# Kernel tuning notes

Hardware: AMD Instinct MI355X
Metric: run time of the kernel (lower is better)

Reference implementation:

```python
import jax, jax.numpy as jnp
import numpy as np

B, T, S, NH, MD, FF, H = 2, 4096, 4096, 16, 64, 128, 4
HD = MD // H
NEG_SLOPE = 0.2
MAX_LOG_SCALE = float(np.log(100.0))  # SwinV2-style clamp on learnable logit scale


def layer_norm(x, g, b, eps=1e-5):
    mu = x.mean(-1, keepdims=True)
    var = ((x - mu) ** 2).mean(-1, keepdims=True)
    return (x - mu) * jax.lax.rsqrt(var + eps) * g + b


def leaky(x):
    return jnp.where(x >= 0, x, NEG_SLOPE * x)


def setup_inputs() -> dict:
    key = jax.random.key(0)
    ks = jax.random.split(key, 16)
    p = lambda i, shape: 0.02 * jax.random.normal(ks[i], shape, jnp.float32)
    return dict(
        x=jax.random.normal(ks[0], (B, S, 1), jnp.float32),
        coords_target=jax.random.uniform(ks[1], (B, T, 2), jnp.float32),
        coords_source=jax.random.uniform(ks[2], (B, S, 2), jnp.float32),
        pe_w1=p(3, (2, FF)), pe_b1=jnp.zeros((FF,), jnp.float32),
        pe_w2=p(4, (FF, MD)), pe_b2=jnp.zeros((MD,), jnp.float32),
        q_w=p(5, (MD, MD)), k_w=p(6, (MD, MD)), v_w=p(7, (1, MD)),
        logit_scale=jnp.zeros((H,), jnp.float32),
        out_w=p(8, (MD, MD)), out_b=jnp.zeros((MD,), jnp.float32),
        nh_w1=p(9, (MD, FF)), nh_b1=jnp.zeros((FF,), jnp.float32),
        nh_w2=p(10, (FF, 1)), nh_b2=jnp.zeros((1,), jnp.float32),
        uf_w1=p(11, (MD * NH, MD * NH)), uf_b1=jnp.zeros((MD * NH,), jnp.float32),
        uf_w2=p(12, (MD * NH, MD * NH)), uf_b2=jnp.zeros((MD * NH,), jnp.float32),
        ln1_g=jnp.ones((MD,), jnp.float32), ln1_b=jnp.zeros((MD,), jnp.float32),
        ln2_g=jnp.ones((MD,), jnp.float32), ln2_b=jnp.zeros((MD,), jnp.float32),
        ln3_g=jnp.ones((MD * NH,), jnp.float32), ln3_b=jnp.zeros((MD * NH,), jnp.float32),
    )


def reference(x, coords_target, coords_source, pe_w1, pe_b1, pe_w2, pe_b2,
              q_w, k_w, v_w, logit_scale, out_w, out_b,
              nh_w1, nh_b1, nh_w2, nh_b2, uf_w1, uf_b1, uf_w2, uf_b2,
              ln1_g, ln1_b, ln2_g, ln2_b, ln3_g, ln3_b):
    # ---- nn_layer: kNN gather of source values per target point ----
    d2 = jnp.sum((coords_target[:, :, None, :] - coords_source[:, None, :, :]) ** 2, -1)  # (B,T,S)
    _, idx = jax.lax.top_k(-d2, NH)  # (B,T,NH) nearest source indices
    gather = jax.vmap(lambda a, i: a[i])
    x_nh = gather(x, idx)                  # (B,T,NH,1)
    cs_nh = gather(coords_source, idx)     # (B,T,NH,2)
    rel = cs_nh - coords_target[:, :, None, :]  # relative coords (B,T,NH,2)

    # ---- relative position embedding MLP (with coordinate transform) ----
    c = jnp.sign(rel) * jnp.log1p(jnp.abs(rel))
    pe = jax.nn.relu(c @ pe_w1 + pe_b1) @ pe_w2 + pe_b2  # (B,T,NH,MD)

    # ---- value projection from raw gathered values (before pe add) ----
    v = x_nh.reshape(B * T, NH, 1) @ v_w  # (BT,NH,MD)

    h = layer_norm(x_nh + pe, ln1_g, ln1_b).reshape(B * T, NH, MD)
    q = h @ q_w
    k = h @ k_w

    # ---- local multi-head attention over the NH neighbors (cosine att w/ learnable logit scale) ----
    qh = q.reshape(B * T, NH, H, HD)
    kh = k.reshape(B * T, NH, H, HD)
    vh = v.reshape(B * T, NH, H, HD)
    qn = qh / (jnp.linalg.norm(qh, axis=-1, keepdims=True) + 1e-12)
    kn = kh / (jnp.linalg.norm(kh, axis=-1, keepdims=True) + 1e-12)
    scale = jnp.exp(jnp.minimum(logit_scale, MAX_LOG_SCALE))  # (H,)
    logits = jnp.einsum('nihd,njhd->nhij', qn, kn) * scale[None, :, None, None]
    att = jax.nn.softmax(logits, axis=-1)
    ao = jnp.einsum('nhij,njhd->nihd', att, vh).reshape(B * T, NH, MD)
    ao = ao @ out_w + out_b

    h = layer_norm(h + ao, ln2_g, ln2_b)
    # per-neighborhood MLP: md -> ff -> 1, broadcast residual add
    m = leaky(leaky(h @ nh_w1 + nh_b1) @ nh_w2 + nh_b2)  # (BT,NH,1)
    h = h + m

    # unfold neighbors into channel dim and run wide MLP
    hu = layer_norm(h.reshape(B, T, NH * MD), ln3_g, ln3_b)
    out = leaky(leaky(hu @ uf_w1 + uf_b1) @ uf_w2 + uf_b2)  # (B,T,NH*MD)
    return out
```

## Files before the change

### kernel.cpp

```cpp
#include <hip/hip_runtime.h>
#include <math.h>

#define B_ 2
#define T_ 4096
#define S_ 4096
#define NH_ 16
#define MD_ 64
#define FF_ 128
#define H_ 4
#define HD_ 16
#define BT_ (B_*T_)

typedef unsigned short u16;
typedef unsigned int u32;
typedef unsigned long long u64;
typedef __attribute__((ext_vector_type(8))) short short8;
typedef __attribute__((ext_vector_type(4))) float f32x4;

__device__ __forceinline__ float wsum64(float v) {
  #pragma unroll
  for (int off = 32; off > 0; off >>= 1) v += __shfl_xor(v, off, 64);
  return v;
}
__device__ __forceinline__ float leaky_(float x) { return x >= 0.f ? x : 0.2f * x; }
__device__ __forceinline__ u16 f2bf(float f) {
  u32 u = __float_as_uint(f);
  return (u16)((u + 0x7fffu + ((u >> 16) & 1u)) >> 16);
}
__device__ __forceinline__ float bf2f(u16 h) { return __uint_as_float((u32)h << 16); }

__device__ __forceinline__ void gload16(const void* g, void* l) {
  __builtin_amdgcn_global_load_lds(
      (const __attribute__((address_space(1))) u32*)g,
      (__attribute__((address_space(3))) u32*)l, 16, 0, 0);
}

__device__ __forceinline__ float dist2_(float2 c, float ctx, float cty) {
  float dx = ctx - c.x, dy = cty - c.y;
  return dx * dx + dy * dy;
}

__global__ __launch_bounds__(256) void k1_knn(
    const float* __restrict__ coords_target, const float* __restrict__ coords_source,
    const float* __restrict__ x, float* __restrict__ xnh, float* __restrict__ rel) {
  __shared__ float2 cs_s[S_];
  __shared__ u64 buf[4][128];
  const int tid = threadIdx.x;
  const int lane = tid & 63;
  const int wave = tid >> 6;
  const int n = blockIdx.x * 4 + wave;
  const int b = n >> 12;
  const float2* cs = (const float2*)coords_source + (size_t)b * S_;
  for (int i = tid; i < S_; i += 256) cs_s[i] = cs[i];
  __syncthreads();

  const float ctx = coords_target[n*2+0], cty = coords_target[n*2+1];

  float lmin = INFINITY;
  for (int kk = 0; kk < 64; ++kk)
    lmin = fminf(lmin, dist2_(cs_s[(kk << 6) | lane], ctx, cty));

  float v = lmin;
  #pragma unroll
  for (int k = 2; k <= 64; k <<= 1) {
    #pragma unroll
    for (int j = k >> 1; j > 0; j >>= 1) {
      float o = __shfl_xor(v, j, 64);
      bool keepmin = (((lane & j) == 0) == ((lane & k) == 0));
      v = keepmin ? fminf(v, o) : fmaxf(v, o);
    }
  }
  const float tau = __shfl(v, 15, 64);

  u64* wbuf = buf[wave];
  int cnt = 0;
  for (int kk = 0; kk < 64; ++kk) {
    int s = (kk << 6) | lane;
    float d2 = dist2_(cs_s[s], ctx, cty);
    bool q = (d2 <= tau);
    u64 mask = __ballot(q);
    if (q) {
      int pos = cnt + __popcll(mask & ((1ull << lane) - 1ull));
      if (pos < 128)
        wbuf[pos] = ((u64)__float_as_uint(d2) << 32) | (u32)s;
    }
    cnt += (int)__popcll(mask);
  }

  int myidx = 0;
  if (cnt >= 16 && cnt <= 128) {
    u64 c0 = (lane < cnt) ? wbuf[lane] : ~0ull;
    u64 c1 = (lane + 64 < cnt) ? wbuf[lane + 64] : ~0ull;
    for (int r = 0; r < 16; ++r) {
      u64 m = c0 < c1 ? c0 : c1;
      #pragma unroll
      for (int off = 32; off > 0; off >>= 1) {
        u64 o = __shfl_xor(m, off, 64);
        m = o < m ? o : m;
      }
      if (lane == r) myidx = (int)(u32)(m & 0xffffffffu);
      if (c0 == m) c0 = ~0ull;
      else if (c1 == m) c1 = ~0ull;
    }
  } else {
    float kd[16]; int ki[16];
    #pragma unroll
    for (int j = 0; j < 16; ++j) { kd[j] = INFINITY; ki[j] = 0x7fffffff; }
    for (int kk = 0; kk < 64; ++kk) {
      int s = (kk << 6) | lane;
      float d2 = dist2_(cs_s[s], ctx, cty);
      if (d2 < kd[15]) {
        float cd = d2; int ci = s;
        #pragma unroll
        for (int j = 0; j < 16; ++j) {
          bool sw = cd < kd[j];
          float td = sw ? kd[j] : cd;  int ti = sw ? ki[j] : ci;
          kd[j]    = sw ? cd : kd[j];  ki[j]    = sw ? ci : ki[j];
          cd = td; ci = ti;
        }
      }
    }
    for (int r = 0; r < 16; ++r) {
      float hd = kd[0]; int hi = ki[0];
      #pragma unroll
      for (int off = 32; off > 0; off >>= 1) {
        float od = __shfl_xor(hd, off, 64); int oi = __shfl_xor(hi, off, 64);
        bool take = (od < hd) || (od == hd && oi < hi);
        hd = take ? od : hd; hi = take ? oi : hi;
      }
      if (kd[0] == hd && ki[0] == hi) {
        #pragma unroll
        for (int j = 0; j < 15; ++j) { kd[j] = kd[j+1]; ki[j] = ki[j+1]; }
        kd[15] = INFINITY; ki[15] = 0x7fffffff;
      }
      if (lane == r) myidx = hi;
    }
  }

  if (lane < 16) {
    float2 c = cs_s[myidx];
    xnh[(size_t)n*NH_ + lane] = x[(size_t)b*S_ + myidx];
    rel[((size_t)n*NH_ + lane)*2 + 0] = c.x - ctx;
    rel[((size_t)n*NH_ + lane)*2 + 1] = c.y - cty;
  }
}

__global__ __launch_bounds__(256) void k2_pe(
    const float* __restrict__ rel, const float* __restrict__ xnh,
    const float* __restrict__ pe_w1, const float* __restrict__ pe_b1,
    const float* __restrict__ pe_w2, const float* __restrict__ pe_b2,
    const float* __restrict__ ln1_g, const float* __restrict__ ln1_b,
    float* __restrict__ h_out) {
  const int lane = threadIdx.x & 63;
  const int wave = threadIdx.x >> 6;
  __shared__ float hid[4][4][128];
  const int row0 = blockIdx.x * 16 + wave * 4;

  float c0[4], c1[4], xn[4];
  #pragma unroll
  for (int rr = 0; rr < 4; ++rr) {
    int row = row0 + rr;
    float r0 = rel[(size_t)row*2+0], r1 = rel[(size_t)row*2+1];
    float a0 = log1pf(fabsf(r0)), a1 = log1pf(fabsf(r1));
    c0[rr] = r0 > 0.f ? a0 : (r0 < 0.f ? -a0 : 0.f);
    c1[rr] = r1 > 0.f ? a1 : (r1 < 0.f ? -a1 : 0.f);
    xn[rr] = xnh[row];
  }
  const float w1a0 = pe_w1[lane],    w1a1 = pe_w1[128+lane], b1a = pe_b1[lane];
  const float w1b0 = pe_w1[64+lane], w1b1 = pe_w1[192+lane], b1b = pe_b1[64+lane];
  #pragma unroll
  for (int rr = 0; rr < 4; ++rr) {
    hid[wave][rr][lane]    = fmaxf(fmaf(c0[rr], w1a0, fmaf(c1[rr], w1a1, b1a)), 0.f);
    hid[wave][rr][lane+64] = fmaxf(fmaf(c0[rr], w1b0, fmaf(c1[rr], w1b1, b1b)), 0.f);
  }
  __syncthreads();

  const float b2 = pe_b2[lane];
  float acc[4] = {b2, b2, b2, b2};
  for (int j = 0; j < 128; ++j) {
    float w2 = pe_w2[(size_t)j*64 + lane];
    #pragma unroll
    for (int rr = 0; rr < 4; ++rr) acc[rr] = fmaf(hid[wave][rr][j], w2, acc[rr]);
  }

  const float g = ln1_g[lane], bb = ln1_b[lane];
  #pragma unroll
  for (int rr = 0; rr < 4; ++rr) {
    float v = xn[rr] + acc[rr];
    float mu = wsum64(v) * (1.f/64.f);
    float d = v - mu;
    float var = wsum64(d*d) * (1.f/64.f);
    h_out[(size_t)(row0+rr)*64 + lane] = d * rsqrtf(var + 1e-5f) * g + bb;
  }
}

#define QKS 66
#define HTS 20
__global__ __launch_bounds__(256) void k3_attn(
    const float* __restrict__ h_in, const float* __restrict__ xnh,
    const float* __restrict__ q_w, const float* __restrict__ k_w,
    const float* __restrict__ v_w, const float* __restrict__ logit_scale,
    const float* __restrict__ out_w, const float* __restrict__ out_b,
    const float* __restrict__ nh_w1, const float* __restrict__ nh_b1,
    const float* __restrict__ nh_w2, const float* __restrict__ nh_b2,
    const float* __restrict__ ln2_g, const float* __restrict__ ln2_b,
    const float* __restrict__ ln3_g, const float* __restrict__ ln3_b,
    u16* __restrict__ hu_hi, u16* __restrict__ hu_lo) {
  const int lane = threadIdx.x & 63;
  const int wave = threadIdx.x >> 6;
  const int n = blockIdx.x * 4 + wave;
  __shared__ float h_t[4][64][HTS];
  __shared__ float q_s[4][16][QKS];
  __shared__ float k_s[4][16][QKS];
  __shared__ float svx_s[4][16][4];

  const float* hb = h_in + (size_t)n * (NH_*MD_);
  float hr[16];
  #pragma unroll
  for (int i = 0; i < 16; ++i) {
    hr[i] = hb[i*64 + lane];
    h_t[wave][lane][i] = hr[i];
  }
  float xv[16];
  #pragma unroll
  for (int i = 0; i < 16; ++i) xv[i] = xnh[(size_t)n*NH_ + i];

  float wvo[4];
  #pragma unroll
  for (int h = 0; h < 4; ++h) {
    float a = 0.f;
    for (int d = 0; d < 16; ++d)
      a = fmaf(v_w[h*16+d], out_w[(size_t)(h*16+d)*64 + lane], a);
    wvo[h] = a;
  }
  __syncthreads();

  float aq[16], ak[16];
  #pragma unroll
  for (int i = 0; i < 16; ++i) { aq[i] = 0.f; ak[i] = 0.f; }
  for (int c = 0; c < 64; ++c) {
    float qc = q_w[(size_t)c*64 + lane];
    float kc = k_w[(size_t)c*64 + lane];
    #pragma unroll
    for (int i4 = 0; i4 < 4; ++i4) {
      float4 hv = *(const float4*)&h_t[wave][c][i4*4];
      aq[i4*4+0] = fmaf(hv.x, qc, aq[i4*4+0]);
      aq[i4*4+1] = fmaf(hv.y, qc, aq[i4*4+1]);
      aq[i4*4+2] = fmaf(hv.z, qc, aq[i4*4+2]);
      aq[i4*4+3] = fmaf(hv.w, qc, aq[i4*4+3]);
      ak[i4*4+0] = fmaf(hv.x, kc, ak[i4*4+0]);
      ak[i4*4+1] = fmaf(hv.y, kc, ak[i4*4+1]);
      ak[i4*4+2] = fmaf(hv.z, kc, ak[i4*4+2]);
      ak[i4*4+3] = fmaf(hv.w, kc, ak[i4*4+3]);
    }
  }
  #pragma unroll
  for (int i = 0; i < 16; ++i) { q_s[wave][i][lane] = aq[i]; k_s[wave][i][lane] = ak[i]; }
  __syncthreads();

  const int h_id = lane >> 4, i_id = lane & 15;
  float qv[16]; float qs = 0.f;
  #pragma unroll
  for (int d = 0; d < 16; ++d) {
    qv[d] = q_s[wave][i_id][h_id*16+d];
    qs = fmaf(qv[d], qv[d], qs);
  }
  const float rq = 1.f / (sqrtf(qs) + 1e-12f);
  const float sc = expf(fminf(logit_scale[h_id], 4.60517019f));
  float lg[16];
  #pragma unroll
  for (int j = 0; j < 16; ++j) {
    float ks = 0.f, dt = 0.f;
    #pragma unroll
    for (int d = 0; d < 16; ++d) {
      float kv = k_s[wave][j][h_id*16+d];
      ks = fmaf(kv, kv, ks);
      dt = fmaf(qv[d], kv, dt);
    }
    lg[j] = dt * rq * (1.f/(sqrtf(ks)+1e-12f)) * sc;
  }
  float mx = lg[0];
  #pragma unroll
  for (int j = 1; j < 16; ++j) mx = fmaxf(mx, lg[j]);
  float se = 0.f, sx = 0.f;
  #pragma unroll
  for (int j = 0; j < 16; ++j) {
    float e = __expf(lg[j] - mx);
    se += e;
    sx = fmaf(e, xv[j], sx);
  }
  svx_s[wave][i_id][h_id] = sx / se;
  __syncthreads();

  const float ob = out_b[lane], g2 = ln2_g[lane], bb2 = ln2_b[lane];
  float h2[16];
  #pragma unroll
  for (int i = 0; i < 16; ++i) {
    float o = ob;
    #pragma unroll
    for (int h = 0; h < 4; ++h) o = fmaf(svx_s[wave][i][h], wvo[h], o);
    float t = hr[i] + o;
    float mu = wsum64(t) * (1.f/64.f);
    float d = t - mu;
    float var = wsum64(d*d) * (1.f/64.f);
    h2[i] = d * rsqrtf(var + 1e-5f) * g2 + bb2;
  }
  #pragma unroll
  for (int i = 0; i < 16; ++i) h_t[wave][lane][i] = h2[i];
  __syncthreads();

  float ha[16], hc[16];
  const float nb1a = nh_b1[lane], nb1b = nh_b1[64+lane];
  #pragma unroll
  for (int i = 0; i < 16; ++i) { ha[i] = nb1a; hc[i] = nb1b; }
  for (int c = 0; c < 64; ++c) {
    float wa = nh_w1[(size_t)c*128 + lane];
    float wb = nh_w1[(size_t)c*128 + 64 + lane];
    #pragma unroll
    for (int i4 = 0; i4 < 4; ++i4) {
      float4 hv = *(const float4*)&h_t[wave][c][i4*4];
      ha[i4*4+0] = fmaf(hv.x, wa, ha[i4*4+0]); hc[i4*4+0] = fmaf(hv.x, wb, hc[i4*4+0]);
      ha[i4*4+1] = fmaf(hv.y, wa, ha[i4*4+1]); hc[i4*4+1] = fmaf(hv.y, wb, hc[i4*4+1]);
      ha[i4*4+2] = fmaf(hv.z, wa, ha[i4*4+2]); hc[i4*4+2] = fmaf(hv.z, wb, hc[i4*4+2]);
      ha[i4*4+3] = fmaf(hv.w, wa, ha[i4*4+3]); hc[i4*4+3] = fmaf(hv.w, wb, hc[i4*4+3]);
    }
  }
  const float w2a = nh_w2[lane], w2b = nh_w2[64+lane], nb2 = nh_b2[0];
  float h3[16]; float s1 = 0.f, s2 = 0.f;
  #pragma unroll
  for (int i = 0; i < 16; ++i) {
    float pa = fmaf(leaky_(ha[i]), w2a, leaky_(hc[i]) * w2b);
    float sm = wsum64(pa);
    float mi = leaky_(sm + nb2);
    float v3 = h2[i] + mi;
    h3[i] = v3; s1 += v3; s2 = fmaf(v3, v3, s2);
  }

  s1 = wsum64(s1); s2 = wsum64(s2);
  float mu = s1 * (1.f/1024.f);
  float var = s2 * (1.f/1024.f) - mu*mu;
  float rs = rsqrtf(var + 1e-5f);
  const size_t base = (size_t)n * 1024;
  #pragma unroll
  for (int i = 0; i < 16; ++i) {
    int cch = i*64 + lane;
    float v = (h3[i] - mu) * rs * ln3_g[cch] + ln3_b[cch];
    u16 hi = f2bf(v);
    hu_hi[base + cch] = hi;
    hu_lo[base + cch] = f2bf(v - bf2f(hi));
  }
}

__global__ __launch_bounds__(256) void k0_wsplit(
    const float* __restrict__ W1, const float* __restrict__ W2,
    u16* __restrict__ T1h, u16* __restrict__ T1l,
    u16* __restrict__ T2h, u16* __restrict__ T2l) {
  __shared__ float t[64][65];
  const float* W = blockIdx.z ? W2 : W1;
  u16* Th = blockIdx.z ? T2h : T1h;
  u16* Tl = blockIdx.z ? T2l : T1l;
  const int bx = blockIdx.x * 64, by = blockIdx.y * 64;
  for (int i = threadIdx.x; i < 64*64; i += 256) {
    int r = i >> 6, c = i & 63;
    t[r][c] = W[(size_t)(bx + r) * 1024 + by + c];
  }
  __syncthreads();
  for (int i = threadIdx.x; i < 64*64; i += 256) {
    int r2 = i >> 6, c2 = i & 63;
    float v = t[c2][r2];
    u16 hi = f2bf(v);
    size_t o = (size_t)(by + r2) * 1024 + bx + c2;
    Th[o] = hi;
    Tl[o] = f2bf(v - bf2f(hi));
  }
}

template<int OUT_BF16>
__global__ __launch_bounds__(256, 2) void k5_gemm(
    const u16* __restrict__ Ah, const u16* __restrict__ Al,
    const u16* __restrict__ Bth, const u16* __restrict__ Btl,
    const float* __restrict__ bias,
    u16* __restrict__ Chi, u16* __restrict__ Clo, float* __restrict__ Cf) {
  __shared__ u16 As[2][128*32];
  __shared__ u16 Bs[2][128*32];
  const int tid = threadIdx.x;
  const int lane = tid & 63;
  const int wave = tid >> 6;
  const int wr = (wave >> 1) * 64, wc = (wave & 1) * 64;
  const int mt = (int)blockIdx.x >> 3, nt = (int)blockIdx.x & 7;
  const int m0 = mt * 128, n0 = nt * 128;

  const int sr = tid >> 2, sk = (tid & 3) * 8;
  const size_t a_off = (size_t)(m0 + sr) * 1024 + sk;
  const size_t b_off = (size_t)(n0 + sr) * 1024 + sk;
  u16* lAh = &As[0][0] + tid * 8;
  u16* lAl = &As[1][0] + tid * 8;
  u16* lBh = &Bs[0][0] + tid * 8;
  u16* lBl = &Bs[1][0] + tid * 8;

  f32x4 acc[4][4];
  #pragma unroll
  for (int i = 0; i < 4; ++i)
    #pragma unroll
    for (int j = 0; j < 4; ++j) acc[i][j] = (f32x4){0.f, 0.f, 0.f, 0.f};

  const int fr = lane & 15, fq = lane >> 4;
  const int aoff = (wr + fr) * 32 + fq * 8;
  const int boff = (wc + fr) * 32 + fq * 8;

  for (int k0 = 0; k0 < 1024; k0 += 32) {
    __syncthreads();
    gload16(Ah  + a_off + k0,             lAh);
    gload16(Ah  + a_off + k0 + 64*1024,   lAh + 64*32);
    gload16(Al  + a_off + k0,             lAl);
    gload16(Al  + a_off + k0 + 64*1024,   lAl + 64*32);
    gload16(Bth + b_off + k0,             lBh);
    gload16(Bth + b_off + k0 + 64*1024,   lBh + 64*32);
    gload16(Btl + b_off + k0,             lBl);
    gload16(Btl + b_off + k0 + 64*1024,   lBl + 64*32);
    __syncthreads();

    short8 ah[4], al[4], bh[4], bl[4];
    #pragma unroll
    for (int i = 0; i < 4; ++i) {
      ah[i] = *(const short8*)&As[0][aoff + i*16*32];
      al[i] = *(const short8*)&As[1][aoff + i*16*32];
      bh[i] = *(const short8*)&Bs[0][boff + i*16*32];
      bl[i] = *(const short8*)&Bs[1][boff + i*16*32];
    }
    #pragma unroll
    for (int mi = 0; mi < 4; ++mi)
      #pragma unroll
      for (int ni = 0; ni < 4; ++ni) {
        acc[mi][ni] = __builtin_amdgcn_mfma_f32_16x16x32_bf16(ah[mi], bh[ni], acc[mi][ni], 0, 0, 0);
        acc[mi][ni] = __builtin_amdgcn_mfma_f32_16x16x32_bf16(ah[mi], bl[ni], acc[mi][ni], 0, 0, 0);
        acc[mi][ni] = __builtin_amdgcn_mfma_f32_16x16x32_bf16(al[mi], bh[ni], acc[mi][ni], 0, 0, 0);
      }
  }

  #pragma unroll
  for (int mi = 0; mi < 4; ++mi)
    #pragma unroll
    for (int ni = 0; ni < 4; ++ni) {
      const int col = n0 + wc + ni*16 + fr;
      const float bv = bias[col];
      #pragma unroll
      for (int r = 0; r < 4; ++r) {
        const int row = m0 + wr + mi*16 + fq*4 + r;
        float v = leaky_(acc[mi][ni][r] + bv);
        if (OUT_BF16) {
          u16 hi = f2bf(v);
          Chi[(size_t)row*1024 + col] = hi;
          Clo[(size_t)row*1024 + col] = f2bf(v - bf2f(hi));
        } else {
          Cf[(size_t)row*1024 + col] = v;
        }
      }
    }
}

extern "C" void kernel_launch(void* const* d_in, const int* in_sizes, int n_in,
                              void* d_out, int out_size, void* d_ws, size_t ws_size,
                              hipStream_t stream) {
  (void)in_sizes; (void)n_in; (void)out_size; (void)ws_size;
  const float* x     = (const float*)d_in[0];
  const float* ct    = (const float*)d_in[1];
  const float* cs    = (const float*)d_in[2];
  const float* pe_w1 = (const float*)d_in[3];
  const float* pe_b1 = (const float*)d_in[4];
  const float* pe_w2 = (const float*)d_in[5];
  const float* pe_b2 = (const float*)d_in[6];
  const float* q_w   = (const float*)d_in[7];
  const float* k_w   = (const float*)d_in[8];
  const float* v_w   = (const float*)d_in[9];
  const float* lsc   = (const float*)d_in[10];
  const float* out_w = (const float*)d_in[11];
  const float* out_b = (const float*)d_in[12];
  const float* nh_w1 = (const float*)d_in[13];
  const float* nh_b1 = (const float*)d_in[14];
  const float* nh_w2 = (const float*)d_in[15];
  const float* nh_b2 = (const float*)d_in[16];
  const float* uf_w1 = (const float*)d_in[17];
  const float* uf_b1 = (const float*)d_in[18];
  const float* uf_w2 = (const float*)d_in[19];
  const float* uf_b2 = (const float*)d_in[20];
  const float* ln1_g = (const float*)d_in[21];
  const float* ln1_b = (const float*)d_in[22];
  const float* ln2_g = (const float*)d_in[23];
  const float* ln2_b = (const float*)d_in[24];
  const float* ln3_g = (const float*)d_in[25];
  const float* ln3_b = (const float*)d_in[26];

  float* ws  = (float*)d_ws;
  float* xnh = ws;
  float* rel = ws + 131072;
  float* h   = ws + 393216;
  u16*  hu_hi = (u16*)(ws + 393216 + 8388608);
  u16*  hu_lo = hu_hi + 8388608;
  u16*  wbase = (u16*)(ws + 393216 + 2*8388608);
  u16*  w1t_hi = wbase;
  u16*  w1t_lo = wbase + 1048576;
  u16*  w2t_hi = wbase + 2*1048576;
  u16*  w2t_lo = wbase + 3*1048576;
  u16*  mid_hi = (u16*)h;
  u16*  mid_lo = mid_hi + 8388608;
  float* out = (float*)d_out;

  k0_wsplit<<<dim3(16, 16, 2), dim3(256), 0, stream>>>(uf_w1, uf_w2,
                                                       w1t_hi, w1t_lo, w2t_hi, w2t_lo);
  k1_knn<<<dim3(BT_/4), dim3(256), 0, stream>>>(ct, cs, x, xnh, rel);
  k2_pe<<<dim3(BT_*NH_/16), dim3(256), 0, stream>>>(rel, xnh, pe_w1, pe_b1, pe_w2, pe_b2,
                                                    ln1_g, ln1_b, h);
  k3_attn<<<dim3(BT_/4), dim3(256), 0, stream>>>(h, xnh, q_w, k_w, v_w, lsc, out_w, out_b,
                                                 nh_w1, nh_b1, nh_w2, nh_b2,
                                                 ln2_g, ln2_b, ln3_g, ln3_b, hu_hi, hu_lo);
  k5_gemm<1><<<dim3(512), dim3(256), 0, stream>>>(hu_hi, hu_lo, w1t_hi, w1t_lo, uf_b1,
                                                  mid_hi, mid_lo, nullptr);
  k5_gemm<0><<<dim3(512), dim3(256), 0, stream>>>(mid_hi, mid_lo, w2t_hi, w2t_lo, uf_b2,
                                                  nullptr, nullptr, out);
}
```

Baseline: 482.4 us.

## Move attention-block Q/K and neighborhood MLP projections onto bf16x3 MFMA

The fp32 FMA loops in k3_attn for the Q/K projections and the neighborhood MLP first layer are replaced by 16x16x32 bf16 MFMA using a hi/lo split (three products per tile) to keep near-fp32 accuracy. A new prep kernel transposes and splits q_w, k_w and nh_w1 into bf16 hi/lo. Work is now shared across the block's four waves: each wave computes one head or one column slice for all four rows, with cross-wave reductions through shared memory. This trades scalar FMA cost for MFMA throughput, at the price of extra block-wide syncs, storing q/k as bf16 (less precision in the cosine logits), and one more kernel launch.

```diff
diff --git a/kernel.cpp b/kernel.cpp
--- a/kernel.cpp
+++ b/kernel.cpp
@@ -194,36 +194,41 @@
   }
 }
 
-#define QKS 66
-#define HTS 20
+#define HBF_S 72
+#define QKS2 24
 __global__ __launch_bounds__(256) void k3_attn(
     const float* __restrict__ h_in, const float* __restrict__ xnh,
-    const float* __restrict__ q_w, const float* __restrict__ k_w,
+    const u16* __restrict__ qkwt_hi, const u16* __restrict__ qkwt_lo,
+    const u16* __restrict__ nhw1t_hi, const u16* __restrict__ nhw1t_lo,
     const float* __restrict__ v_w, const float* __restrict__ logit_scale,
     const float* __restrict__ out_w, const float* __restrict__ out_b,
-    const float* __restrict__ nh_w1, const float* __restrict__ nh_b1,
-    const float* __restrict__ nh_w2, const float* __restrict__ nh_b2,
+    const float* __restrict__ nh_b1, const float* __restrict__ nh_w2,
+    const float* __restrict__ nh_b2,
     const float* __restrict__ ln2_g, const float* __restrict__ ln2_b,
     const float* __restrict__ ln3_g, const float* __restrict__ ln3_b,
     u16* __restrict__ hu_hi, u16* __restrict__ hu_lo) {
-  const int lane = threadIdx.x & 63;
-  const int wave = threadIdx.x >> 6;
+  const int tid = threadIdx.x;
+  const int lane = tid & 63;
+  const int wave = tid >> 6;
   const int n = blockIdx.x * 4 + wave;
-  __shared__ float h_t[4][64][HTS];
-  __shared__ float q_s[4][16][QKS];
-  __shared__ float k_s[4][16][QKS];
+
+  __shared__ u16 h_bf[2][64][HBF_S];
+  __shared__ u16 q_s[4][64][QKS2];
+  __shared__ u16 k_s[4][64][QKS2];
+  __shared__ float xnh_s[64];
   __shared__ float svx_s[4][16][4];
+  __shared__ float mred[4][64];
 
   const float* hb = h_in + (size_t)n * (NH_*MD_);
   float hr[16];
   #pragma unroll
   for (int i = 0; i < 16; ++i) {
     hr[i] = hb[i*64 + lane];
-    h_t[wave][lane][i] = hr[i];
-  }
-  float xv[16];
-  #pragma unroll
-  for (int i = 0; i < 16; ++i) xv[i] = xnh[(size_t)n*NH_ + i];
+    u16 hi16 = f2bf(hr[i]);
+    h_bf[0][wave*16 + i][lane] = hi16;
+    h_bf[1][wave*16 + i][lane] = f2bf(hr[i] - bf2f(hi16));
+  }
+  if (tid < 64) xnh_s[tid] = xnh[(size_t)blockIdx.x * 64 + tid];
 
   float wvo[4];
   #pragma unroll
@@ -235,61 +240,85 @@
   }
   __syncthreads();
 
-  float aq[16], ak[16];
-  #pragma unroll
-  for (int i = 0; i < 16; ++i) { aq[i] = 0.f; ak[i] = 0.f; }
-  for (int c = 0; c < 64; ++c) {
-    float qc = q_w[(size_t)c*64 + lane];
-    float kc = k_w[(size_t)c*64 + lane];
-    #pragma unroll
-    for (int i4 = 0; i4 < 4; ++i4) {
-      float4 hv = *(const float4*)&h_t[wave][c][i4*4];
-      aq[i4*4+0] = fmaf(hv.x, qc, aq[i4*4+0]);
-      aq[i4*4+1] = fmaf(hv.y, qc, aq[i4*4+1]);
-      aq[i4*4+2] = fmaf(hv.z, qc, aq[i4*4+2]);
-      aq[i4*4+3] = fmaf(hv.w, qc, aq[i4*4+3]);
-      ak[i4*4+0] = fmaf(hv.x, kc, ak[i4*4+0]);
-      ak[i4*4+1] = fmaf(hv.y, kc, ak[i4*4+1]);
-      ak[i4*4+2] = fmaf(hv.z, kc, ak[i4*4+2]);
-      ak[i4*4+3] = fmaf(hv.w, kc, ak[i4*4+3]);
-    }
-  }
-  #pragma unroll
-  for (int i = 0; i < 16; ++i) { q_s[wave][i][lane] = aq[i]; k_s[wave][i][lane] = ak[i]; }
-  __syncthreads();
-
-  const int h_id = lane >> 4, i_id = lane & 15;
-  float qv[16]; float qs = 0.f;
-  #pragma unroll
-  for (int d = 0; d < 16; ++d) {
-    qv[d] = q_s[wave][i_id][h_id*16+d];
-    qs = fmaf(qv[d], qv[d], qs);
-  }
-  const float rq = 1.f / (sqrtf(qs) + 1e-12f);
-  const float sc = expf(fminf(logit_scale[h_id], 4.60517019f));
-  float lg[16];
-  #pragma unroll
-  for (int j = 0; j < 16; ++j) {
-    float ks = 0.f, dt = 0.f;
-    #pragma unroll
-    for (int d = 0; d < 16; ++d) {
-      float kv = k_s[wave][j][h_id*16+d];
-      ks = fmaf(kv, kv, ks);
-      dt = fmaf(qv[d], kv, dt);
-    }
-    lg[j] = dt * rq * (1.f/(sqrtf(ks)+1e-12f)) * sc;
-  }
-  float mx = lg[0];
-  #pragma unroll
-  for (int j = 1; j < 16; ++j) mx = fmaxf(mx, lg[j]);
-  float se = 0.f, sx = 0.f;
-  #pragma unroll
-  for (int j = 0; j < 16; ++j) {
-    float e = __expf(lg[j] - mx);
-    se += e;
-    sx = fmaf(e, xv[j], sx);
-  }
-  svx_s[wave][i_id][h_id] = sx / se;
+  const int fr = lane & 15, fq = lane >> 4;
+  {
+    short8 bqh[2], bql[2], bkh[2], bkl[2];
+    #pragma unroll
+    for (int ks = 0; ks < 2; ++ks) {
+      const int qcol = wave*16 + fr, kcol = 64 + wave*16 + fr;
+      const int ko = ks*32 + fq*8;
+      bqh[ks] = *(const short8*)&qkwt_hi[qcol*64 + ko];
+      bql[ks] = *(const short8*)&qkwt_lo[qcol*64 + ko];
+      bkh[ks] = *(const short8*)&qkwt_hi[kcol*64 + ko];
+      bkl[ks] = *(const short8*)&qkwt_lo[kcol*64 + ko];
+    }
+    f32x4 accq[4], acck[4];
+    #pragma unroll
+    for (int mf = 0; mf < 4; ++mf) { accq[mf] = (f32x4){0,0,0,0}; acck[mf] = (f32x4){0,0,0,0}; }
+    #pragma unroll
+    for (int ks = 0; ks < 2; ++ks) {
+      #pragma unroll
+      for (int mf = 0; mf < 4; ++mf) {
+        short8 ah = *(const short8*)&h_bf[0][mf*16 + fr][ks*32 + fq*8];
+        short8 al = *(const short8*)&h_bf[1][mf*16 + fr][ks*32 + fq*8];
+        accq[mf] = __builtin_amdgcn_mfma_f32_16x16x32_bf16(ah, bqh[ks], accq[mf], 0,0,0);
+        accq[mf] = __builtin_amdgcn_mfma_f32_16x16x32_bf16(ah, bql[ks], accq[mf], 0,0,0);
+        accq[mf] = __builtin_amdgcn_mfma_f32_16x16x32_bf16(al, bqh[ks], accq[mf], 0,0,0);
+        acck[mf] = __builtin_amdgcn_mfma_f32_16x16x32_bf16(ah, bkh[ks], acck[mf], 0,0,0);
+        acck[mf] = __builtin_amdgcn_mfma_f32_16x16x32_bf16(ah, bkl[ks], acck[mf], 0,0,0);
+        acck[mf] = __builtin_amdgcn_mfma_f32_16x16x32_bf16(al, bkh[ks], acck[mf], 0,0,0);
+      }
+    }
+    #pragma unroll
+    for (int mf = 0; mf < 4; ++mf)
+      #pragma unroll
+      for (int r = 0; r < 4; ++r) {
+        const int row = mf*16 + fq*4 + r;
+        q_s[wave][row][fr] = f2bf(accq[mf][r]);
+        k_s[wave][row][fr] = f2bf(acck[mf][r]);
+      }
+  }
+  __syncthreads();
+
+  {
+    const int nl = lane >> 4, il = lane & 15;
+    const float sc = expf(fminf(logit_scale[wave], 4.60517019f));
+    float qv[16]; float qs = 0.f;
+    short8 qp0 = *(const short8*)&q_s[wave][lane][0];
+    short8 qp1 = *(const short8*)&q_s[wave][lane][8];
+    #pragma unroll
+    for (int d = 0; d < 8; ++d) {
+      qv[d]   = bf2f((u16)qp0[d]);  qs = fmaf(qv[d],   qv[d],   qs);
+      qv[8+d] = bf2f((u16)qp1[d]);  qs = fmaf(qv[8+d], qv[8+d], qs);
+    }
+    const float rq = 1.f / (sqrtf(qs) + 1e-12f);
+    float lg[16];
+    #pragma unroll
+    for (int j = 0; j < 16; ++j) {
+      short8 kp0 = *(const short8*)&k_s[wave][(lane & 48) + j][0];
+      short8 kp1 = *(const short8*)&k_s[wave][(lane & 48) + j][8];
+      float ks = 0.f, dt = 0.f;
+      #pragma unroll
+      for (int d = 0; d < 8; ++d) {
+        float kv0 = bf2f((u16)kp0[d]);
+        float kv1 = bf2f((u16)kp1[d]);
+        ks = fmaf(kv0, kv0, ks); dt = fmaf(qv[d], kv0, dt);
+        ks = fmaf(kv1, kv1, ks); dt = fmaf(qv[8+d], kv1, dt);
+      }
+      lg[j] = dt * rq * (1.f/(sqrtf(ks)+1e-12f)) * sc;
+    }
+    float mx = lg[0];
+    #pragma unroll
+    for (int j = 1; j < 16; ++j) mx = fmaxf(mx, lg[j]);
+    float se = 0.f, sx = 0.f;
+    #pragma unroll
+    for (int j = 0; j < 16; ++j) {
+      float e = __expf(lg[j] - mx);
+      se += e;
+      sx = fmaf(e, xnh_s[(lane & 48) + j], sx);
+    }
+    svx_s[nl][il][wave] = sx / se;
+  }
   __syncthreads();
 
   const float ob = out_b[lane], g2 = ln2_g[lane], bb2 = ln2_b[lane];
@@ -306,36 +335,70 @@
     h2[i] = d * rsqrtf(var + 1e-5f) * g2 + bb2;
   }
   #pragma unroll
-  for (int i = 0; i < 16; ++i) h_t[wave][lane][i] = h2[i];
-  __syncthreads();
-
-  float ha[16], hc[16];
-  const float nb1a = nh_b1[lane], nb1b = nh_b1[64+lane];
-  #pragma unroll
-  for (int i = 0; i < 16; ++i) { ha[i] = nb1a; hc[i] = nb1b; }
-  for (int c = 0; c < 64; ++c) {
-    float wa = nh_w1[(size_t)c*128 + lane];
-    float wb = nh_w1[(size_t)c*128 + 64 + lane];
-    #pragma unroll
-    for (int i4 = 0; i4 < 4; ++i4) {
-      float4 hv = *(const float4*)&h_t[wave][c][i4*4];
-      ha[i4*4+0] = fmaf(hv.x, wa, ha[i4*4+0]); hc[i4*4+0] = fmaf(hv.x, wb, hc[i4*4+0]);
-      ha[i4*4+1] = fmaf(hv.y, wa, ha[i4*4+1]); hc[i4*4+1] = fmaf(hv.y, wb, hc[i4*4+1]);
-      ha[i4*4+2] = fmaf(hv.z, wa, ha[i4*4+2]); hc[i4*4+2] = fmaf(hv.z, wb, hc[i4*4+2]);
-      ha[i4*4+3] = fmaf(hv.w, wa, ha[i4*4+3]); hc[i4*4+3] = fmaf(hv.w, wb, hc[i4*4+3]);
-    }
-  }
-  const float w2a = nh_w2[lane], w2b = nh_w2[64+lane], nb2 = nh_b2[0];
-  float h3[16]; float s1 = 0.f, s2 = 0.f;
-  #pragma unroll
   for (int i = 0; i < 16; ++i) {
-    float pa = fmaf(leaky_(ha[i]), w2a, leaky_(hc[i]) * w2b);
-    float sm = wsum64(pa);
+    u16 hi16 = f2bf(h2[i]);
+    h_bf[0][wave*16 + i][lane] = hi16;
+    h_bf[1][wave*16 + i][lane] = f2bf(h2[i] - bf2f(hi16));
+  }
+  __syncthreads();
+
+  {
+    short8 bnh[2][2], bnl[2][2];
+    float b1v[2], w2v[2];
+    #pragma unroll
+    for (int cf = 0; cf < 2; ++cf) {
+      const int col = wave*32 + cf*16 + fr;
+      b1v[cf] = nh_b1[col];
+      w2v[cf] = nh_w2[col];
+      #pragma unroll
+      for (int ks = 0; ks < 2; ++ks) {
+        bnh[cf][ks] = *(const short8*)&nhw1t_hi[col*64 + ks*32 + fq*8];
+        bnl[cf][ks] = *(const short8*)&nhw1t_lo[col*64 + ks*32 + fq*8];
+      }
+    }
+    f32x4 accm[4][2];
+    #pragma unroll
+    for (int mf = 0; mf < 4; ++mf)
+      #pragma unroll
+      for (int cf = 0; cf < 2; ++cf) accm[mf][cf] = (f32x4){0,0,0,0};
+    #pragma unroll
+    for (int ks = 0; ks < 2; ++ks) {
+      #pragma unroll
+      for (int mf = 0; mf < 4; ++mf) {
+        short8 ah = *(const short8*)&h_bf[0][mf*16 + fr][ks*32 + fq*8];
+        short8 al = *(const short8*)&h_bf[1][mf*16 + fr][ks*32 + fq*8];
+        #pragma unroll
+        for (int cf = 0; cf < 2; ++cf) {
+          accm[mf][cf] = __builtin_amdgcn_mfma_f32_16x16x32_bf16(ah, bnh[cf][ks], accm[mf][cf], 0,0,0);
+          accm[mf][cf] = __builtin_amdgcn_mfma_f32_16x16x32_bf16(ah, bnl[cf][ks], accm[mf][cf], 0,0,0);
+          accm[mf][cf] = __builtin_amdgcn_mfma_f32_16x16x32_bf16(al, bnh[cf][ks], accm[mf][cf], 0,0,0);
+        }
+      }
+    }
+    #pragma unroll
+    for (int mf = 0; mf < 4; ++mf)
+      #pragma unroll
+      for (int r = 0; r < 4; ++r) {
+        float p = leaky_(accm[mf][0][r] + b1v[0]) * w2v[0]
+                + leaky_(accm[mf][1][r] + b1v[1]) * w2v[1];
+        #pragma unroll
+        for (int off = 1; off < 16; off <<= 1) p += __shfl_xor(p, off, 64);
+        if (fr == 0) mred[wave][mf*16 + fq*4 + r] = p;
+      }
+  }
+  __syncthreads();
+
+  const float nb2 = nh_b2[0];
+  float s1 = 0.f, s2 = 0.f;
+  #pragma unroll
+  for (int i = 0; i < 16; ++i) {
+    float sm = mred[0][wave*16+i] + mred[1][wave*16+i]
+             + mred[2][wave*16+i] + mred[3][wave*16+i];
     float mi = leaky_(sm + nb2);
     float v3 = h2[i] + mi;
-    h3[i] = v3; s1 += v3; s2 = fmaf(v3, v3, s2);
-  }
-
+    hr[i] = v3;
+    s1 += v3; s2 = fmaf(v3, v3, s2);
+  }
   s1 = wsum64(s1); s2 = wsum64(s2);
   float mu = s1 * (1.f/1024.f);
   float var = s2 * (1.f/1024.f) - mu*mu;
@@ -344,10 +407,10 @@
   #pragma unroll
   for (int i = 0; i < 16; ++i) {
     int cch = i*64 + lane;
-    float v = (h3[i] - mu) * rs * ln3_g[cch] + ln3_b[cch];
-    u16 hi = f2bf(v);
-    hu_hi[base + cch] = hi;
-    hu_lo[base + cch] = f2bf(v - bf2f(hi));
+    float v = (hr[i] - mu) * rs * ln3_g[cch] + ln3_b[cch];
+    u16 hi16 = f2bf(v);
+    hu_hi[base + cch] = hi16;
+    hu_lo[base + cch] = f2bf(v - bf2f(hi16));
   }
 }
 
@@ -372,6 +435,27 @@
     size_t o = (size_t)(by + r2) * 1024 + bx + c2;
     Th[o] = hi;
     Tl[o] = f2bf(v - bf2f(hi));
+  }
+}
+
+__global__ __launch_bounds__(256) void k0b_wsplit2(
+    const float* __restrict__ q_w, const float* __restrict__ k_w,
+    const float* __restrict__ nh_w1,
+    u16* __restrict__ qkwt_hi, u16* __restrict__ qkwt_lo,
+    u16* __restrict__ nhw1t_hi, u16* __restrict__ nhw1t_lo) {
+  int idx = blockIdx.x * 256 + threadIdx.x;
+  int e = idx & 8191;
+  int col = e >> 6, kk = e & 63;
+  if (idx < 8192) {
+    float v = (col < 64) ? q_w[kk*64 + col] : k_w[kk*64 + (col - 64)];
+    u16 hi = f2bf(v);
+    qkwt_hi[col*64 + kk] = hi;
+    qkwt_lo[col*64 + kk] = f2bf(v - bf2f(hi));
+  } else {
+    float v = nh_w1[kk*128 + col];
+    u16 hi = f2bf(v);
+    nhw1t_hi[col*64 + kk] = hi;
+    nhw1t_lo[col*64 + kk] = f2bf(v - bf2f(hi));
   }
 }
 
@@ -502,17 +586,25 @@
   u16*  w1t_lo = wbase + 1048576;
   u16*  w2t_hi = wbase + 2*1048576;
   u16*  w2t_lo = wbase + 3*1048576;
+  u16*  qkwt_hi  = wbase + 4*1048576;
+  u16*  qkwt_lo  = qkwt_hi + 8192;
+  u16*  nhw1t_hi = qkwt_hi + 16384;
+  u16*  nhw1t_lo = qkwt_hi + 24576;
   u16*  mid_hi = (u16*)h;
   u16*  mid_lo = mid_hi + 8388608;
   float* out = (float*)d_out;
 
   k0_wsplit<<<dim3(16, 16, 2), dim3(256), 0, stream>>>(uf_w1, uf_w2,
                                                        w1t_hi, w1t_lo, w2t_hi, w2t_lo);
+  k0b_wsplit2<<<dim3(64), dim3(256), 0, stream>>>(q_w, k_w, nh_w1,
+                                                  qkwt_hi, qkwt_lo, nhw1t_hi, nhw1t_lo);
   k1_knn<<<dim3(BT_/4), dim3(256), 0, stream>>>(ct, cs, x, xnh, rel);
   k2_pe<<<dim3(BT_*NH_/16), dim3(256), 0, stream>>>(rel, xnh, pe_w1, pe_b1, pe_w2, pe_b2,
                                                     ln1_g, ln1_b, h);
-  k3_attn<<<dim3(BT_/4), dim3(256), 0, stream>>>(h, xnh, q_w, k_w, v_w, lsc, out_w, out_b,
-                                                 nh_w1, nh_b1, nh_w2, nh_b2,
+  k3_attn<<<dim3(BT_/4), dim3(256), 0, stream>>>(h, xnh, qkwt_hi, qkwt_lo,
+                                                 nhw1t_hi, nhw1t_lo,
+                                                 v_w, lsc, out_w, out_b,
+                                                 nh_b1, nh_w2, nh_b2,
                                                  ln2_g, ln2_b, ln3_g, ln3_b, hu_hi, hu_lo);
   k5_gemm<1><<<dim3(512), dim3(256), 0, stream>>>(hu_hi, hu_lo, w1t_hi, w1t_lo, uf_b1,
                                                   mid_hi, mid_lo, nullptr);
```

New measurement: 466.5 us. 1.03x faster.
